# Performance work log

Hardware: AMD Instinct MI355X
Metric: run time of the kernel (lower is better)

The kernel has to match this reference:

```python
import jax, jax.numpy as jnp
import numpy as np

TK, HA = 3, 8          # num_blocks, num_heads
AVGF = 32              # num_submatrices
LN_EPS = 1e-5


def _layernorm(x, g, b):
    m = jnp.mean(x, axis=-1, keepdims=True)
    v = jnp.mean((x - m) ** 2, axis=-1, keepdims=True)
    return (x - m) / jnp.sqrt(v + LN_EPS) * g + b


def setup_inputs() -> dict:
    key = jax.random.key(0)
    ks = jax.random.split(key, 12)
    A, B, T = 16, 128, 512
    M = A * B              # 2048
    Dh = M // HA           # 256
    H = 4 * M              # 8192
    s = 0.05               # scale randn params so activations stay finite
    return {
        "x": jax.random.normal(ks[0], (A, B, T), jnp.float32),
        "weight": jax.random.normal(ks[1], (M, M), jnp.float32) * s,
        "Wq": jax.random.normal(ks[2], (TK, HA, Dh, M), jnp.float32) * s,
        "Wk": jax.random.normal(ks[3], (TK, HA, Dh, M), jnp.float32) * s,
        "Wv": jax.random.normal(ks[4], (TK, HA, Dh, M), jnp.float32) * s,
        "Wo": jax.random.normal(ks[5], (TK, M, M), jnp.float32) * s,
        "ln1_g": jnp.ones((M,), jnp.float32),
        "ln1_b": jnp.zeros((M,), jnp.float32),
        "ln2_g": jnp.ones((M,), jnp.float32),
        "ln2_b": jnp.zeros((M,), jnp.float32),
        "fc1_w": jax.random.normal(ks[6], (H, M), jnp.float32) * 0.02,
        "fc1_b": jnp.zeros((H,), jnp.float32),
        "fc2_w": jax.random.normal(ks[7], (M, H), jnp.float32) * 0.02,
        "fc2_b": jnp.zeros((M,), jnp.float32),
    }


def reference(x, weight, Wq, Wk, Wv, Wo, ln1_g, ln1_b, ln2_g, ln2_b,
              fc1_w, fc1_b, fc2_w, fc2_b):
    A, B, T = x.shape
    M = A * B
    Dh = M // HA
    seg = T // AVGF
    # redefine(): transpose(0,2) -> (T,B,A), segment-average along time, flatten
    xt = jnp.transpose(x, (2, 1, 0))                       # (T, B, A)
    xc = xt.reshape(AVGF, seg, B, A).mean(axis=1)          # (AVGF, B, A)
    xcf = xc.reshape(AVGF, M)                              # (AVGF, M)
    # savespace[i] = weight @ x[i]  + sinusoidal positional bias
    pos = jnp.arange(AVGF, dtype=jnp.float32)[:, None]
    je = jnp.arange(0, M, 2, dtype=jnp.float32)
    ang = pos / (10000.0 ** (2.0 * je / M))                # (AVGF, M/2)
    bias = jnp.zeros((AVGF, M), jnp.float32)
    bias = bias.at[:, 0::2].set(jnp.sin(ang)).at[:, 1::2].set(jnp.cos(ang))
    s0 = xcf @ weight.T + bias                             # (AVGF, M)
    scale = 1.0 / jnp.sqrt(jnp.float32(Dh))

    # Sequential recurrence over tokens: vcum[a] carries the cumulative
    # softmax-weighted V sum (softmax over a scalar == 1) per block/head.
    def step(vcum, s):
        for a in range(TK):
            xn = _layernorm(s, ln1_g, ln1_b)
            q = jnp.einsum('hdm,m->hd', Wq[a], xn)         # (HA, Dh)
            k = jnp.einsum('hdm,m->hd', Wk[a], xn)
            v = jnp.einsum('hdm,m->hd', Wv[a], xn)
            scores = jnp.sum(q * k, axis=-1) * scale       # (HA,) scalars
            w = jax.nn.softmax(scores[:, None], axis=-1)[:, 0]  # ones
            vcum = vcum.at[a].add(w[:, None] * v)
            s = Wo[a] @ vcum[a].reshape(-1) + s
            s = _layernorm(s, ln2_g, ln2_b) + s
            h = jax.nn.gelu(fc1_w @ s + fc1_b, approximate=False)
            s = fc2_w @ h + fc2_b
        return vcum, s

    vcum0 = jnp.zeros((TK, HA, Dh), s0.dtype)
    _, out = jax.lax.scan(step, vcum0, s0)                 # (AVGF, M)
    return out.reshape(AVGF, B, A)
```

## Files before the change

### kernel.cpp

```cpp
#include <hip/hip_runtime.h>
#include <math.h>

typedef __attribute__((ext_vector_type(8))) short short8;
typedef __attribute__((ext_vector_type(4))) float floatx4;

__device__ inline unsigned f2bf1(float f) {
    union { float f; unsigned u; } v; v.f = f;
    return (v.u + 0x8000u) >> 16;
}

__device__ inline short8 pack8(float4 a, float4 b) {
    short8 r;
    r[0] = (short)f2bf1(a.x); r[1] = (short)f2bf1(a.y);
    r[2] = (short)f2bf1(a.z); r[3] = (short)f2bf1(a.w);
    r[4] = (short)f2bf1(b.x); r[5] = (short)f2bf1(b.y);
    r[6] = (short)f2bf1(b.z); r[7] = (short)f2bf1(b.w);
    return r;
}

__device__ inline float gelu1(float x) {
    return 0.5f * x * (1.0f + erff(x * 0.70710678118654752f));
}

__global__ __launch_bounds__(128) void avg_k(const float* __restrict__ x,
                                             float* __restrict__ xcf) {
    int blk = blockIdx.x;
    int a = blk >> 7, b = blk & 127;
    int t = threadIdx.x;
    const float4 v = *(const float4*)(x + ((size_t)a * 128 + b) * 512 + t * 4);
    float s = v.x + v.y + v.z + v.w;
    s += __shfl_xor(s, 1);
    s += __shfl_xor(s, 2);
    if ((t & 3) == 0) {
        int seg = t >> 2;
        xcf[seg * 2048 + b * 16 + a] = s * (1.0f / 16.0f);
    }
}

__global__ __launch_bounds__(256) void stats_k(const float* __restrict__ Sin,
                                               float* __restrict__ st) {
    __shared__ float red[8];
    const int row = blockIdx.x, t = threadIdx.x;
    const float* xr = Sin + (size_t)row * 2048;
    float4 v0 = *(const float4*)(xr + t * 4);
    float4 v1 = *(const float4*)(xr + 1024 + t * 4);
    float s = v0.x + v0.y + v0.z + v0.w + v1.x + v1.y + v1.z + v1.w;
    for (int o = 32; o; o >>= 1) s += __shfl_down(s, o);
    if ((t & 63) == 0) red[t >> 6] = s;
    __syncthreads();
    float mean = (red[0] + red[1] + red[2] + red[3]) * (1.0f / 2048.0f);
    float d0 = v0.x - mean, d1 = v0.y - mean, d2 = v0.z - mean, d3 = v0.w - mean;
    float e0 = v1.x - mean, e1 = v1.y - mean, e2 = v1.z - mean, e3 = v1.w - mean;
    float s2 = d0*d0 + d1*d1 + d2*d2 + d3*d3 + e0*e0 + e1*e1 + e2*e2 + e3*e3;
    for (int o = 32; o; o >>= 1) s2 += __shfl_down(s2, o);
    if ((t & 63) == 0) red[4 + (t >> 6)] = s2;
    __syncthreads();
    if (t == 0) {
        float var = (red[4] + red[5] + red[6] + red[7]) * (1.0f / 2048.0f);
        st[row * 2]     = mean;
        st[row * 2 + 1] = 1.0f / sqrtf(var + 1e-5f);
    }
}

template<int KCHUNK, int STAGE, int EPI>
__global__ __launch_bounds__(256) void gemm_k(const float* __restrict__ X,
                                              const float* __restrict__ W,
                                              float* __restrict__ C,
                                              const float* __restrict__ ebias,
                                              const float* __restrict__ stats,
                                              const float* __restrict__ sg,
                                              const float* __restrict__ sb,
                                              int N, int K) {
    constexpr int PITCH = KCHUNK + 8;
    __shared__ unsigned short Xs[32 * PITCH];
    const int tid = threadIdx.x;
    const int bx = blockIdx.x, by = blockIdx.y;
    const int kb0 = by * KCHUNK;
    const int w = tid >> 6, lane = tid & 63;
    const int q = lane >> 4, r16 = lane & 15;
    const int nb = bx * 64 + w * 16;

    constexpr int KI = KCHUNK / 32;
    const float* wp0 = W + (size_t)(nb + r16) * K + kb0 + q * 8;
    float4 wr0[KI], wr1[KI];
#pragma unroll
    for (int ki = 0; ki < KI; ki++) {
        wr0[ki] = *(const float4*)(wp0 + ki * 32);
        wr1[ki] = *(const float4*)(wp0 + ki * 32 + 4);
    }

    if constexpr (STAGE == 2) {
        for (int c = tid; c < KCHUNK; c += 256) {
            const float* vp = X + kb0 + c;
            float run = 0.f;
#pragma unroll
            for (int r = 0; r < 32; r++) {
                run += vp[(size_t)r * K];
                Xs[r * PITCH + c] = (unsigned short)f2bf1(run);
            }
        }
    } else {
        constexpr int NF4 = 32 * (KCHUNK / 4);
        for (int f = tid; f < NF4; f += 256) {
            const int row = f / (KCHUNK / 4), c4 = f % (KCHUNK / 4);
            const int k0 = kb0 + c4 * 4;
            float4 v = *(const float4*)(X + (size_t)row * K + k0);
            if constexpr (STAGE == 1 || STAGE == 11) {
                const float m = stats[row * 2], rs = stats[row * 2 + 1];
                const float4 gg = *(const float4*)(sg + k0);
                const float4 bb = *(const float4*)(sb + k0);
                float4 o;
                o.x = (v.x - m) * rs * gg.x + bb.x;
                o.y = (v.y - m) * rs * gg.y + bb.y;
                o.z = (v.z - m) * rs * gg.z + bb.z;
                o.w = (v.w - m) * rs * gg.w + bb.w;
                if constexpr (STAGE == 11) {
                    o.x += v.x; o.y += v.y; o.z += v.z; o.w += v.w;
                }
                v = o;
            }
            if constexpr (STAGE == 3) {
                const float4 bb = *(const float4*)(sg + k0);
                v.x = gelu1(v.x + bb.x);
                v.y = gelu1(v.y + bb.y);
                v.z = gelu1(v.z + bb.z);
                v.w = gelu1(v.w + bb.w);
            }
            ushort4 p;
            p.x = (unsigned short)f2bf1(v.x);
            p.y = (unsigned short)f2bf1(v.y);
            p.z = (unsigned short)f2bf1(v.z);
            p.w = (unsigned short)f2bf1(v.w);
            *(ushort4*)&Xs[row * PITCH + c4 * 4] = p;
        }
    }
    __syncthreads();

    floatx4 acc0 = {}, acc1 = {};
#pragma unroll
    for (int ki = 0; ki < KI; ki++) {
        short8 a0 = *(const short8*)&Xs[r16 * PITCH + ki * 32 + q * 8];
        short8 a1 = *(const short8*)&Xs[(16 + r16) * PITCH + ki * 32 + q * 8];
        short8 bf = pack8(wr0[ki], wr1[ki]);
        acc0 = __builtin_amdgcn_mfma_f32_16x16x32_bf16(a0, bf, acc0, 0, 0, 0);
        acc1 = __builtin_amdgcn_mfma_f32_16x16x32_bf16(a1, bf, acc1, 0, 0, 0);
    }

#pragma unroll
    for (int mt = 0; mt < 2; mt++)
#pragma unroll
        for (int e = 0; e < 4; e++) {
            int i = mt * 16 + q * 4 + e;
            int n = nb + r16;
            float v = (mt == 0) ? acc0[e] : acc1[e];
            if (EPI == 1 && by == 0) v += ebias[n];
            if (EPI == 2 && by == 0) {
                int ne = n & ~1;
                float ang = (float)i * __expf(-(float)ne * (9.210340371976184f / 1024.0f));
                v += (n & 1) ? cosf(ang) : sinf(ang);
            }
            atomicAdd(C + (size_t)i * N + n, v);
        }
}

extern "C" void kernel_launch(void* const* d_in, const int* in_sizes, int n_in,
                              void* d_out, int out_size, void* d_ws, size_t ws_size,
                              hipStream_t stream) {
    const float* x      = (const float*)d_in[0];
    const float* weight = (const float*)d_in[1];
    const float* Wv     = (const float*)d_in[4];
    const float* Wo     = (const float*)d_in[5];
    const float* ln1g   = (const float*)d_in[6];
    const float* ln1b   = (const float*)d_in[7];
    const float* ln2g   = (const float*)d_in[8];
    const float* ln2b   = (const float*)d_in[9];
    const float* fc1w   = (const float*)d_in[10];
    const float* fc1b   = (const float*)d_in[11];
    const float* fc2w   = (const float*)d_in[12];
    const float* fc2b   = (const float*)d_in[13];
    float* ws  = (float*)d_ws;
    float* xcf = ws;
    float* S   = ws + 65536;
    float* V   = ws + 131072;
    float* H   = ws + 196608;
    float* st1 = ws + 458752;
    float* st2 = ws + 458816;
    float* out = (float*)d_out;

    avg_k<<<2048, 128, 0, stream>>>(x, xcf);

    hipMemsetAsync(S, 0, 65536 * 4, stream);
    gemm_k<64, 0, 2><<<dim3(32, 32), 256, 0, stream>>>(
        xcf, weight, S, nullptr, nullptr, nullptr, nullptr, 2048, 2048);

    for (int a = 0; a < 3; a++) {
        stats_k<<<32, 256, 0, stream>>>(S, st1);
        hipMemsetAsync(V, 0, (65536 + 262144) * 4, stream);
        gemm_k<64, 1, 0><<<dim3(32, 32), 256, 0, stream>>>(
            S, Wv + (size_t)a * 4194304, V, nullptr, st1, ln1g, ln1b, 2048, 2048);
        gemm_k<64, 2, 0><<<dim3(32, 32), 256, 0, stream>>>(
            V, Wo + (size_t)a * 4194304, S, nullptr, nullptr, nullptr, nullptr, 2048, 2048);
        stats_k<<<32, 256, 0, stream>>>(S, st2);
        gemm_k<128, 11, 0><<<dim3(128, 16), 256, 0, stream>>>(
            S, fc1w, H, nullptr, st2, ln2g, ln2b, 8192, 2048);
        float* Co = (a == 2) ? out : S;
        hipMemsetAsync(Co, 0, 65536 * 4, stream);
        gemm_k<128, 3, 1><<<dim3(32, 64), 256, 0, stream>>>(
            H, fc2w, Co, fc2b, nullptr, fc1b, nullptr, 2048, 8192);
    }
}
```

Measured before the change: 484.3 us.

## Reduce split-K within 1024-thread blocks and move V prefix-sum after Wo GEMM

The small-M GEMM kernel is restructured. Each of 16 waves in a 1024-thread block now handles its own K slice, loading and converting activations straight from global memory, and the partial sums are reduced in LDS before a single atomic (or plain store) per output. This replaces many 256-thread blocks that each issued atomics for every output element, cutting atomic traffic and removing the activation staging in shared memory. The cumulative sum over V is moved after the Wo projection using linearity, done by a separate cumadd kernel. The fc1 GEMM now covers full K per block and writes without atomics. The risks are fewer blocks with little per-wave load parallelism, and redundant activation reads through cache.

```diff
diff --git a/kernel.cpp b/kernel.cpp
--- a/kernel.cpp
+++ b/kernel.cpp
@@ -20,6 +20,25 @@
 
 __device__ inline float gelu1(float x) {
     return 0.5f * x * (1.0f + erff(x * 0.70710678118654752f));
+}
+
+__device__ inline float4 lnmap(float4 v, float m, float rs, float4 g, float4 b, int addres) {
+    float4 o;
+    o.x = (v.x - m) * rs * g.x + b.x;
+    o.y = (v.y - m) * rs * g.y + b.y;
+    o.z = (v.z - m) * rs * g.z + b.z;
+    o.w = (v.w - m) * rs * g.w + b.w;
+    if (addres) { o.x += v.x; o.y += v.y; o.z += v.z; o.w += v.w; }
+    return o;
+}
+
+__device__ inline float4 gelmap(float4 v, float4 b) {
+    float4 o;
+    o.x = gelu1(v.x + b.x);
+    o.y = gelu1(v.y + b.y);
+    o.z = gelu1(v.z + b.z);
+    o.w = gelu1(v.w + b.w);
+    return o;
 }
 
 __global__ __launch_bounds__(128) void avg_k(const float* __restrict__ x,
@@ -62,105 +81,103 @@
     }
 }
 
-template<int KCHUNK, int STAGE, int EPI>
-__global__ __launch_bounds__(256) void gemm_k(const float* __restrict__ X,
-                                              const float* __restrict__ W,
-                                              float* __restrict__ C,
-                                              const float* __restrict__ ebias,
-                                              const float* __restrict__ stats,
-                                              const float* __restrict__ sg,
-                                              const float* __restrict__ sb,
-                                              int N, int K) {
-    constexpr int PITCH = KCHUNK + 8;
-    __shared__ unsigned short Xs[32 * PITCH];
+__global__ __launch_bounds__(256) void cumadd_k(const float* __restrict__ U,
+                                                float* __restrict__ S) {
+    int c = blockIdx.x * 256 + threadIdx.x;
+    float run = 0.f;
+#pragma unroll
+    for (int r = 0; r < 32; r++) {
+        run += U[r * 2048 + c];
+        S[r * 2048 + c] += run;
+    }
+}
+
+template<int KPW, int STAGE, int EPI, int ATOM>
+__global__ __launch_bounds__(1024, 4) void gemm_k(const float* __restrict__ X,
+                                                  const float* __restrict__ W,
+                                                  float* __restrict__ C,
+                                                  const float* __restrict__ ebias,
+                                                  const float* __restrict__ stats,
+                                                  const float* __restrict__ sg,
+                                                  const float* __restrict__ sb,
+                                                  int N, int K) {
+    __shared__ float red[16 * 512];
     const int tid = threadIdx.x;
-    const int bx = blockIdx.x, by = blockIdx.y;
-    const int kb0 = by * KCHUNK;
     const int w = tid >> 6, lane = tid & 63;
     const int q = lane >> 4, r16 = lane & 15;
-    const int nb = bx * 64 + w * 16;
-
-    constexpr int KI = KCHUNK / 32;
-    const float* wp0 = W + (size_t)(nb + r16) * K + kb0 + q * 8;
-    float4 wr0[KI], wr1[KI];
-#pragma unroll
-    for (int ki = 0; ki < KI; ki++) {
-        wr0[ki] = *(const float4*)(wp0 + ki * 32);
-        wr1[ki] = *(const float4*)(wp0 + ki * 32 + 4);
-    }
-
-    if constexpr (STAGE == 2) {
-        for (int c = tid; c < KCHUNK; c += 256) {
-            const float* vp = X + kb0 + c;
-            float run = 0.f;
-#pragma unroll
-            for (int r = 0; r < 32; r++) {
-                run += vp[(size_t)r * K];
-                Xs[r * PITCH + c] = (unsigned short)f2bf1(run);
-            }
-        }
-    } else {
-        constexpr int NF4 = 32 * (KCHUNK / 4);
-        for (int f = tid; f < NF4; f += 256) {
-            const int row = f / (KCHUNK / 4), c4 = f % (KCHUNK / 4);
-            const int k0 = kb0 + c4 * 4;
-            float4 v = *(const float4*)(X + (size_t)row * K + k0);
-            if constexpr (STAGE == 1 || STAGE == 11) {
-                const float m = stats[row * 2], rs = stats[row * 2 + 1];
-                const float4 gg = *(const float4*)(sg + k0);
-                const float4 bb = *(const float4*)(sb + k0);
-                float4 o;
-                o.x = (v.x - m) * rs * gg.x + bb.x;
-                o.y = (v.y - m) * rs * gg.y + bb.y;
-                o.z = (v.z - m) * rs * gg.z + bb.z;
-                o.w = (v.w - m) * rs * gg.w + bb.w;
-                if constexpr (STAGE == 11) {
-                    o.x += v.x; o.y += v.y; o.z += v.z; o.w += v.w;
-                }
-                v = o;
-            }
-            if constexpr (STAGE == 3) {
-                const float4 bb = *(const float4*)(sg + k0);
-                v.x = gelu1(v.x + bb.x);
-                v.y = gelu1(v.y + bb.y);
-                v.z = gelu1(v.z + bb.z);
-                v.w = gelu1(v.w + bb.w);
-            }
-            ushort4 p;
-            p.x = (unsigned short)f2bf1(v.x);
-            p.y = (unsigned short)f2bf1(v.y);
-            p.z = (unsigned short)f2bf1(v.z);
-            p.w = (unsigned short)f2bf1(v.w);
-            *(ushort4*)&Xs[row * PITCH + c4 * 4] = p;
+    const int nb = blockIdx.x * 16;
+    const int kb0 = (blockIdx.y * 16 + w) * KPW;
+
+    const float* wp  = W + (size_t)(nb + r16) * K + kb0 + q * 8;
+    const float* xp0 = X + (size_t)r16 * K + kb0 + q * 8;
+    const float* xp1 = X + (size_t)(16 + r16) * K + kb0 + q * 8;
+
+    float m0 = 0.f, rs0 = 0.f, m1 = 0.f, rs1 = 0.f;
+    if constexpr (STAGE == 1 || STAGE == 11) {
+        m0 = stats[r16 * 2];        rs0 = stats[r16 * 2 + 1];
+        m1 = stats[(16 + r16) * 2]; rs1 = stats[(16 + r16) * 2 + 1];
+    }
+
+    floatx4 acc0 = {}, acc1 = {};
+#pragma unroll
+    for (int ks = 0; ks < KPW; ks += 32) {
+        const int k0 = kb0 + ks + q * 8;
+        float4 w0  = *(const float4*)(wp + ks);
+        float4 w1  = *(const float4*)(wp + ks + 4);
+        float4 x00 = *(const float4*)(xp0 + ks);
+        float4 x01 = *(const float4*)(xp0 + ks + 4);
+        float4 x10 = *(const float4*)(xp1 + ks);
+        float4 x11 = *(const float4*)(xp1 + ks + 4);
+        if constexpr (STAGE == 1 || STAGE == 11) {
+            const float4 g0 = *(const float4*)(sg + k0);
+            const float4 g1 = *(const float4*)(sg + k0 + 4);
+            const float4 b0 = *(const float4*)(sb + k0);
+            const float4 b1 = *(const float4*)(sb + k0 + 4);
+            const int ar = (STAGE == 11);
+            x00 = lnmap(x00, m0, rs0, g0, b0, ar);
+            x01 = lnmap(x01, m0, rs0, g1, b1, ar);
+            x10 = lnmap(x10, m1, rs1, g0, b0, ar);
+            x11 = lnmap(x11, m1, rs1, g1, b1, ar);
+        }
+        if constexpr (STAGE == 3) {
+            const float4 c0 = *(const float4*)(sg + k0);
+            const float4 c1 = *(const float4*)(sg + k0 + 4);
+            x00 = gelmap(x00, c0);
+            x01 = gelmap(x01, c1);
+            x10 = gelmap(x10, c0);
+            x11 = gelmap(x11, c1);
+        }
+        short8 bw = pack8(w0, w1);
+        short8 a0 = pack8(x00, x01);
+        short8 a1 = pack8(x10, x11);
+        acc0 = __builtin_amdgcn_mfma_f32_16x16x32_bf16(a0, bw, acc0, 0, 0, 0);
+        acc1 = __builtin_amdgcn_mfma_f32_16x16x32_bf16(a1, bw, acc1, 0, 0, 0);
+    }
+
+    {
+        const int base = w * 512 + q * 64 + r16;
+#pragma unroll
+        for (int e = 0; e < 4; e++) {
+            red[base + e * 16]       = acc0[e];
+            red[base + 256 + e * 16] = acc1[e];
         }
     }
     __syncthreads();
-
-    floatx4 acc0 = {}, acc1 = {};
-#pragma unroll
-    for (int ki = 0; ki < KI; ki++) {
-        short8 a0 = *(const short8*)&Xs[r16 * PITCH + ki * 32 + q * 8];
-        short8 a1 = *(const short8*)&Xs[(16 + r16) * PITCH + ki * 32 + q * 8];
-        short8 bf = pack8(wr0[ki], wr1[ki]);
-        acc0 = __builtin_amdgcn_mfma_f32_16x16x32_bf16(a0, bf, acc0, 0, 0, 0);
-        acc1 = __builtin_amdgcn_mfma_f32_16x16x32_bf16(a1, bf, acc1, 0, 0, 0);
-    }
-
-#pragma unroll
-    for (int mt = 0; mt < 2; mt++)
-#pragma unroll
-        for (int e = 0; e < 4; e++) {
-            int i = mt * 16 + q * 4 + e;
-            int n = nb + r16;
-            float v = (mt == 0) ? acc0[e] : acc1[e];
-            if (EPI == 1 && by == 0) v += ebias[n];
-            if (EPI == 2 && by == 0) {
-                int ne = n & ~1;
-                float ang = (float)i * __expf(-(float)ne * (9.210340371976184f / 1024.0f));
-                v += (n & 1) ? cosf(ang) : sinf(ang);
-            }
-            atomicAdd(C + (size_t)i * N + n, v);
-        }
+    if (tid < 512) {
+        float v = 0.f;
+#pragma unroll
+        for (int ww = 0; ww < 16; ww++) v += red[ww * 512 + tid];
+        const int i = tid >> 4;
+        const int n = nb + (tid & 15);
+        if (EPI == 1 && blockIdx.y == 0) v += ebias[n];
+        if (EPI == 2 && blockIdx.y == 0) {
+            int ne = n & ~1;
+            float ang = (float)i * __expf(-(float)ne * (9.210340371976184f / 1024.0f));
+            v += (n & 1) ? cosf(ang) : sinf(ang);
+        }
+        if constexpr (ATOM) atomicAdd(C + (size_t)i * N + n, v);
+        else                C[(size_t)i * N + n] = v;
+    }
 }
 
 extern "C" void kernel_launch(void* const* d_in, const int* in_sizes, int n_in,
@@ -182,30 +199,32 @@
     float* xcf = ws;
     float* S   = ws + 65536;
     float* V   = ws + 131072;
-    float* H   = ws + 196608;
-    float* st1 = ws + 458752;
-    float* st2 = ws + 458816;
+    float* U   = ws + 196608;
+    float* H   = ws + 262144;
+    float* st1 = ws + 524288;
+    float* st2 = ws + 524352;
     float* out = (float*)d_out;
 
     avg_k<<<2048, 128, 0, stream>>>(x, xcf);
 
     hipMemsetAsync(S, 0, 65536 * 4, stream);
-    gemm_k<64, 0, 2><<<dim3(32, 32), 256, 0, stream>>>(
+    gemm_k<64, 0, 2, 1><<<dim3(128, 2), 1024, 0, stream>>>(
         xcf, weight, S, nullptr, nullptr, nullptr, nullptr, 2048, 2048);
 
     for (int a = 0; a < 3; a++) {
         stats_k<<<32, 256, 0, stream>>>(S, st1);
-        hipMemsetAsync(V, 0, (65536 + 262144) * 4, stream);
-        gemm_k<64, 1, 0><<<dim3(32, 32), 256, 0, stream>>>(
+        hipMemsetAsync(V, 0, 131072 * 4, stream);
+        gemm_k<64, 1, 0, 1><<<dim3(128, 2), 1024, 0, stream>>>(
             S, Wv + (size_t)a * 4194304, V, nullptr, st1, ln1g, ln1b, 2048, 2048);
-        gemm_k<64, 2, 0><<<dim3(32, 32), 256, 0, stream>>>(
-            V, Wo + (size_t)a * 4194304, S, nullptr, nullptr, nullptr, nullptr, 2048, 2048);
+        gemm_k<64, 0, 0, 1><<<dim3(128, 2), 1024, 0, stream>>>(
+            V, Wo + (size_t)a * 4194304, U, nullptr, nullptr, nullptr, nullptr, 2048, 2048);
+        cumadd_k<<<8, 256, 0, stream>>>(U, S);
         stats_k<<<32, 256, 0, stream>>>(S, st2);
-        gemm_k<128, 11, 0><<<dim3(128, 16), 256, 0, stream>>>(
+        gemm_k<128, 11, 0, 0><<<dim3(512, 1), 1024, 0, stream>>>(
             S, fc1w, H, nullptr, st2, ln2g, ln2b, 8192, 2048);
         float* Co = (a == 2) ? out : S;
         hipMemsetAsync(Co, 0, 65536 * 4, stream);
-        gemm_k<128, 3, 1><<<dim3(32, 64), 256, 0, stream>>>(
+        gemm_k<256, 3, 1, 1><<<dim3(128, 2), 1024, 0, stream>>>(
             H, fc2w, Co, fc2b, nullptr, fc1b, nullptr, 2048, 8192);
     }
 }
```

Result: slower. 531.1 us (+9.7%).
